# Performance work log

Hardware: AMD Instinct MI355X
Metric: run time of the kernel (lower is better)

## Reference

```python
import jax, jax.numpy as jnp
import numpy as np

NUM_HEADS = 8
NSCALE = 2  # len(sr_ratio) + 1 with sr_ratio=[2.0]


def setup_inputs() -> dict:
    key = jax.random.key(0)
    ks = jax.random.split(key, 12)
    B, Nq, Np, C, n_up, N_all = 16, 1024, 1024, 512, 2048, 4096
    s = C ** -0.5  # keep attention logits in a sane range
    return {
        "query": jax.random.normal(ks[0], (Nq, B, C), jnp.float32),
        "key": jax.random.normal(ks[1], (Np, B, C), jnp.float32),
        "key_pos": jax.random.uniform(ks[2], (B, Np, 3), jnp.float32),
        "xyz_all": jax.random.uniform(ks[3], (B, N_all, 3), jnp.float32),
        "xyz_upsample": jax.random.uniform(ks[4], (B, n_up, 3), jnp.float32),
        "Wq": jax.random.normal(ks[5], (C, C), jnp.float32) * s,
        "Wkv1": jax.random.normal(ks[6], (C, C), jnp.float32) * s,
        "Wkv2": jax.random.normal(ks[7], (C, C), jnp.float32) * s,
        "fp_w": jax.random.normal(ks[8], (C, C), jnp.float32) * s,
        "fp_b": jnp.zeros((C,), jnp.float32),
        "proj_w": jax.random.normal(ks[9], (C, C), jnp.float32) * s,
        "proj_b": jnp.zeros((C,), jnp.float32),
    }


def _fp_upsample(xyz_up, key_pos, key_feats, fp_w, fp_b):
    """PointnetFPModuleUpSample: 3-NN inverse-distance feature interpolation
    from Np known points (key_pos) onto n_up target points, followed by a
    pointwise MLP (1x1 conv, BN folded) + ReLU.
    key_feats: (Np, B, C) -> returns (B, n_up, C)."""
    d2 = jnp.sum((xyz_up[:, :, None, :] - key_pos[:, None, :, :]) ** 2, axis=-1)  # (B, n, Np)
    negd, idx = jax.lax.top_k(-d2, 3)  # 3 nearest neighbors, (B, n, 3)
    w = 1.0 / (-negd + 1e-8)
    w = w / jnp.sum(w, axis=-1, keepdims=True)
    feats = jnp.transpose(key_feats, (1, 0, 2))  # (B, Np, C)
    g = jnp.take_along_axis(feats[:, None, :, :], idx[..., None], axis=2)  # (B, n, 3, C)
    interp = jnp.sum(g * w[..., None], axis=2)  # (B, n, C)
    return jax.nn.relu(interp @ fp_w.T + fp_b)


def reference(query, key, key_pos, xyz_all, xyz_upsample,
              Wq, Wkv1, Wkv2, fp_w, fp_b, proj_w, proj_b):
    Np, B, C = key.shape
    Nq = query.shape[0]
    H = NUM_HEADS
    nh = H // NSCALE  # heads per scale group
    hd = C // H
    scale = hd ** -0.5

    # NOTE: torch reshapes (N,B,C) -> (B,N,...) WITHOUT permuting first; we
    # replicate the identical row-major reshape for bit-faithful structure.
    q = (query @ Wq.T).reshape(B, Nq, H, hd).transpose(0, 2, 1, 3)  # (B,H,Nq,hd)

    def attend(qs, kv):
        k, v = kv[0], kv[1]
        a = jax.nn.softmax(jnp.einsum('bhqd,bhkd->bhqk', qs, k) * scale, axis=-1)
        o = jnp.einsum('bhqk,bhkd->bhqd', a, v)
        return o.transpose(0, 2, 1, 3).reshape(B, Nq, nh * hd)

    # scale 1: full-resolution keys
    kv1 = (key @ Wkv1.T).reshape(B, -1, 2, nh, hd).transpose(2, 0, 3, 1, 4)
    x1 = attend(q[:, :nh], kv1)

    # scale 2: FP-upsampled keys (sr_ratio=2.0 -> 2*base_np points)
    key2 = _fp_upsample(xyz_upsample, key_pos, key, fp_w, fp_b)  # (B, n, C)
    key2_nbc = key2.transpose(1, 0, 2)  # (n, B, C), matches permute(2,0,1) of (B,C,n)
    kv2 = (key2_nbc @ Wkv2.T).reshape(B, -1, 2, nh, hd).transpose(2, 0, 3, 1, 4)
    x2 = attend(q[:, nh:], kv2)

    x = jnp.concatenate([x1, x2], axis=-1) @ proj_w.T + proj_b  # (B, Nq, C)
    return x.transpose(1, 0, 2)  # (Nq, B, C)
```

## Files before the change

### kernel.cpp

```cpp
#include <hip/hip_runtime.h>
#include <cstdint>
#include <cstddef>

#define CD   512
#define BDIM 16
#define NQ   1024
#define NP   1024
#define NUP  2048

typedef unsigned short u16;
typedef short short8 __attribute__((ext_vector_type(8)));
typedef float f32x4  __attribute__((ext_vector_type(4)));
typedef uint32_t u32x4 __attribute__((ext_vector_type(4)));

#define GLOAD16(g, l) __builtin_amdgcn_global_load_lds( \
    (const __attribute__((address_space(1))) void*)(g), \
    (__attribute__((address_space(3))) void*)(l), 16, 0, 0)

__device__ __forceinline__ u16 rne_bf16(float x) {
  uint32_t u = __float_as_uint(x);
  return (u16)((u + 0x7fffu + ((u >> 16) & 1u)) >> 16);
}
__device__ __forceinline__ float bf2f(u16 v) {
  return __uint_as_float(((uint32_t)v) << 16);
}

__global__ __launch_bounds__(256) void prep_kernel(
    const float* __restrict__ query, u16* __restrict__ Qa,
    const float* __restrict__ key, u16* __restrict__ Ka,
    const float* __restrict__ Wq, const float* __restrict__ Wkv1,
    const float* __restrict__ projw, const float* __restrict__ fpw,
    const float* __restrict__ wkv2, u16* __restrict__ Wq2,
    u16* __restrict__ Wkv12, u16* __restrict__ proj2,
    u16* __restrict__ fpwb, u16* __restrict__ wkv2b,
    const float* __restrict__ key_pos, const float* __restrict__ xyz_up,
    int* __restrict__ idx_out, float* __restrict__ w_out)
{
  const int bx = blockIdx.x;
  const int tid = threadIdx.x;
  if (bx < 8832) {
    const float* in; u16* out; float scl = 1.0f; long u;
    if (bx < 8192) {
      in = (bx < 4096) ? query : key;
      out = (bx < 4096) ? Qa : Ka;
      u = (long)(bx & 4095) * 256 + tid;
    } else {
      const int job = (bx - 8192) >> 7;
      in  = (job == 0) ? Wq  : (job == 1) ? Wkv1  : (job == 2) ? projw : (job == 3) ? fpw  : wkv2;
      out = (job == 0) ? Wq2 : (job == 1) ? Wkv12 : (job == 2) ? proj2 : (job == 3) ? fpwb : wkv2b;
      if (job == 0) scl = 0.18033688011112042f;
      u = (long)((bx - 8192) & 127) * 256 + tid;
    }
    const float* ip = in + u * 8;
    float v[8];
    *(float4*)&v[0] = *(const float4*)ip;
    *(float4*)&v[4] = *(const float4*)(ip + 4);
    short8 o;
#pragma unroll
    for (int i = 0; i < 8; ++i) o[i] = (short)rne_bf16(v[i] * scl);
    *(short8*)(out + u * 8) = o;
    return;
  }
  __shared__ __align__(16) float4 kp4[NP];
  const int kb = bx - 8832;
  const int b = kb >> 7;
  const int n0 = (kb & 127) * 16;
  const float* kpb = key_pos + (long)b * NP * 3;
#pragma unroll
  for (int s = 0; s < 4; ++s) {
    const int t = s * 256 + tid;
    kp4[t] = make_float4(kpb[t * 3], kpb[t * 3 + 1], kpb[t * 3 + 2], 0.0f);
  }
  __syncthreads();
  const int sc = tid & 15, pt = tid >> 4;
  const int n = n0 + pt;
  const float ux = xyz_up[(b * NUP + n) * 3 + 0];
  const float uy = xyz_up[(b * NUP + n) * 3 + 1];
  const float uz = xyz_up[(b * NUP + n) * 3 + 2];
  float e0 = 3.4e38f, e1 = 3.4e38f, e2 = 3.4e38f;
  int j0 = 0, j1 = 0, j2 = 0;
  for (int it = 0; it < 64; ++it) {
    const int j = it * 16 + sc;
    const float4 kv = kp4[j];
    const float dx = ux - kv.x, dy = uy - kv.y, dz = uz - kv.z;
    const float dd = dx * dx + dy * dy + dz * dz;
    if (dd < e2) {
      if (dd < e1) {
        e2 = e1; j2 = j1;
        if (dd < e0) { e1 = e0; j1 = j0; e0 = dd; j0 = j; }
        else         { e1 = dd; j1 = j; }
      } else { e2 = dd; j2 = j; }
    }
  }
#pragma unroll
  for (int ms = 1; ms <= 8; ms <<= 1) {
    const float pd0 = __shfl_xor(e0, ms), pd1 = __shfl_xor(e1, ms), pd2 = __shfl_xor(e2, ms);
    const int   pi0 = __shfl_xor(j0, ms), pi1 = __shfl_xor(j1, ms), pi2 = __shfl_xor(j2, ms);
    float cd[3] = {pd0, pd1, pd2};
    int   ci[3] = {pi0, pi1, pi2};
#pragma unroll
    for (int t = 0; t < 3; ++t) {
      const float dd = cd[t]; const int jj = ci[t];
      if (dd < e2 || (dd == e2 && jj < j2)) {
        if (dd < e1 || (dd == e1 && jj < j1)) {
          e2 = e1; j2 = j1;
          if (dd < e0 || (dd == e0 && jj < j0)) { e1 = e0; j1 = j0; e0 = dd; j0 = jj; }
          else                                  { e1 = dd; j1 = jj; }
        } else { e2 = dd; j2 = jj; }
      }
    }
  }
  if (sc == 0) {
    const float w0 = 1.0f / (e0 + 1e-8f);
    const float w1 = 1.0f / (e1 + 1e-8f);
    const float w2 = 1.0f / (e2 + 1e-8f);
    const float inv = 1.0f / ((w0 + w1) + w2);
    const long r = (long)b * NUP + n;
    idx_out[r * 3 + 0] = j0; idx_out[r * 3 + 1] = j1; idx_out[r * 3 + 2] = j2;
    w_out[r * 3 + 0] = w0 * inv; w_out[r * 3 + 1] = w1 * inv; w_out[r * 3 + 2] = w2 * inv;
  }
}

__global__ __launch_bounds__(256) void interp_bf16_kernel(
    const u16* __restrict__ Ka, const int* __restrict__ idx,
    const float* __restrict__ w, u16* __restrict__ out)
{
  const int t = threadIdx.x;
  const long r = (long)blockIdx.x * 4 + (t >> 6);
  const int j = t & 63;
  const int b = (int)(r >> 11);
  const int j0 = idx[r * 3 + 0], j1 = idx[r * 3 + 1], j2 = idx[r * 3 + 2];
  const float w0 = w[r * 3 + 0], w1 = w[r * 3 + 1], w2 = w[r * 3 + 2];
  const short8 a0 = *(const short8*)(Ka + ((long)j0 * BDIM + b) * CD + j * 8);
  const short8 a1 = *(const short8*)(Ka + ((long)j1 * BDIM + b) * CD + j * 8);
  const short8 a2 = *(const short8*)(Ka + ((long)j2 * BDIM + b) * CD + j * 8);
  short8 o;
#pragma unroll
  for (int i = 0; i < 8; ++i)
    o[i] = (short)rne_bf16(bf2f((u16)a0[i]) * w0 + bf2f((u16)a1[i]) * w1
                         + bf2f((u16)a2[i]) * w2);
  *(short8*)(out + r * CD + j * 8) = o;
}

template<int AMODE, int OMODE, int KE>
__device__ __forceinline__ void gemm_body64(
    u16* __restrict__ As, u16* __restrict__ Ws,
    const u16* __restrict__ A, const u16* __restrict__ W,
    const float* __restrict__ bias, void* __restrict__ outv,
    const int m0, const int n0)
{
  const int tid = threadIdx.x;
  const int lane = tid & 63, wv = tid >> 6;
  const int rch = tid & 7;

  f32x4 acc[4][4];
#pragma unroll
  for (int mi = 0; mi < 4; ++mi)
#pragma unroll
    for (int ni = 0; ni < 4; ++ni)
#pragma unroll
      for (int r = 0; r < 4; ++r) acc[mi][ni][r] = 0.0f;

  const long rowb = (long)KE * 2;
  const char* gA[4]; const char* gW[4];
#pragma unroll
  for (int s = 0; s < 4; ++s) {
    const int row = s * 32 + (tid >> 3);
    const int gm = m0 + row;
    const long arow = (AMODE == 0) ? (long)gm : (long)(gm & 15) * 2048 + (gm >> 4);
    const int kb0 = (rch ^ (row & 7)) << 4;
    gA[s] = (const char*)A + arow * rowb + kb0;
    gW[s] = (const char*)W + (long)(n0 + row) * rowb + kb0;
  }
  const int wr = (wv >> 1) * 64, wc = (wv & 1) * 64;
  const int g = lane >> 4, cl = lane & 15;

  for (int kt = 0; kt < KE / 64; ++kt) {
#pragma unroll
    for (int s = 0; s < 4; ++s) {
      GLOAD16(gA[s], (char*)As + (s * 256 + tid) * 16);
      GLOAD16(gW[s], (char*)Ws + (s * 256 + tid) * 16);
      gA[s] += 128; gW[s] += 128;
    }
    __syncthreads();
#pragma unroll
    for (int kb = 0; kb < 2; ++kb) {
      short8 af[4], bf[4];
#pragma unroll
      for (int i = 0; i < 4; ++i) {
        const int ra = wr + i * 16 + cl;
        af[i] = *(const short8*)((const char*)As + ra * 128
                 + ((kb * 64 + g * 16) ^ ((ra & 7) << 4)));
        const int rb = wc + i * 16 + cl;
        bf[i] = *(const short8*)((const char*)Ws + rb * 128
                 + ((kb * 64 + g * 16) ^ ((rb & 7) << 4)));
      }
#pragma unroll
      for (int mi = 0; mi < 4; ++mi)
#pragma unroll
        for (int ni = 0; ni < 4; ++ni)
          acc[mi][ni] = __builtin_amdgcn_mfma_f32_16x16x32_bf16(af[mi], bf[ni], acc[mi][ni], 0, 0, 0);
    }
    __syncthreads();
  }

#pragma unroll
  for (int mi = 0; mi < 4; ++mi)
#pragma unroll
    for (int ni = 0; ni < 4; ++ni)
#pragma unroll
      for (int r = 0; r < 4; ++r) {
        const int gm = m0 + wr + mi * 16 + g * 4 + r;
        const int gn = n0 + wc + ni * 16 + cl;
        float v = acc[mi][ni][r];
        if (OMODE == 0) {
          ((u16*)outv)[(long)gm * 512 + gn] = rne_bf16(v);
        } else if (OMODE == 1) {
          v = fmaxf(v + bias[gn], 0.0f);
          ((u16*)outv)[(long)gm * 512 + gn] = rne_bf16(v);
        } else {
          v += bias[gn];
          ((float*)outv)[((long)(gm & 1023) * BDIM + (gm >> 10)) * 512 + gn] = v;
        }
      }
}

__global__ __launch_bounds__(256) void gemm_mega_kernel(
    const u16* __restrict__ IN2, const u16* __restrict__ fpwb,
    const float* __restrict__ fp_b, u16* __restrict__ KEY2,
    const u16* __restrict__ Qa, const u16* __restrict__ Wq2, u16* __restrict__ Qb,
    const u16* __restrict__ Ka, const u16* __restrict__ Wkv12, u16* __restrict__ KV1)
{
  __shared__ __align__(16) u16 As[128 * 64];
  __shared__ __align__(16) u16 Ws[128 * 64];
  const int bid = blockIdx.x;
  if (bid < 1024) {
    gemm_body64<0, 1, 512>(As, Ws, IN2, fpwb, fp_b, KEY2, (bid >> 2) * 128, (bid & 3) * 128);
  } else if (bid < 1536) {
    const int t = bid - 1024;
    gemm_body64<0, 0, 512>(As, Ws, Qa, Wq2, nullptr, Qb, (t >> 2) * 128, (t & 3) * 128);
  } else {
    const int t = bid - 1536;
    gemm_body64<0, 0, 512>(As, Ws, Ka, Wkv12, nullptr, KV1, (t >> 2) * 128, (t & 3) * 128);
  }
}

__device__ __forceinline__ void transpose_body(
    u16* __restrict__ L, const u16* __restrict__ KV, u16* __restrict__ Vt,
    const int NK, const int kt, const int h, const int b)
{
  const int t = threadIdx.x;
  {
    const int n = t >> 2, d0 = (t & 3) * 16;
    const u16* src = KV + ((size_t)b * NK + kt * 64 + n) * 512 + 256 + h * 64 + d0;
    *(short8*)&L[n * 68 + d0] = *(const short8*)src;
    *(short8*)&L[n * 68 + d0 + 8] = *(const short8*)(src + 8);
  }
  __syncthreads();
  const int d = t >> 2, n0 = (t & 3) * 16;
  short8 o0, o1;
#pragma unroll
  for (int i = 0; i < 8; ++i) {
    o0[i] = (short)L[(n0 + i) * 68 + d];
    o1[i] = (short)L[(n0 + 8 + i) * 68 + d];
  }
  u16* dst = Vt + ((size_t)((b * 4 + h) * 64 + d)) * NK + kt * 64 + n0;
  *(short8*)dst = o0; *(short8*)(dst + 8) = o1;
}

__global__ __launch_bounds__(256) void gemm_kv2_vt1_kernel(
    const u16* __restrict__ KEY2, const u16* __restrict__ wkv2b,
    u16* __restrict__ KV2,
    const u16* __restrict__ KV1, u16* __restrict__ Vt1)
{
  __shared__ __align__(16) u16 As[128 * 64];
  __shared__ __align__(16) u16 Ws[128 * 64];
  const int bid = blockIdx.x;
  if (bid < 1024) {
    gemm_body64<1, 0, 512>(As, Ws, KEY2, wkv2b, nullptr, KV2,
                           (bid >> 2) * 128, (bid & 3) * 128);
  } else {
    const int tb = bid - 1024;
    transpose_body(As, KV1, Vt1, 1024, tb & 15, (tb >> 4) & 3, tb >> 6);
  }
}

__global__ __launch_bounds__(256) void vt2_kernel(
    const u16* __restrict__ KV2, u16* __restrict__ Vt2)
{
  __shared__ u16 L[64 * 68];
  transpose_body(L, KV2, Vt2, 2048, blockIdx.x, blockIdx.y, blockIdx.z);
}

__global__ __launch_bounds__(256) void gemm_proj64_kernel(
    const u16* __restrict__ A, const u16* __restrict__ W,
    const float* __restrict__ bias, float* __restrict__ out)
{
  __shared__ __align__(16) u16 As[64 * 32];
  __shared__ __align__(16) u16 Ws[128 * 32];
  const int tid = threadIdx.x;
  const int lane = tid & 63, wv = tid >> 6;
  const int m0 = blockIdx.x * 64, n0 = blockIdx.y * 128;

  f32x4 acc[2][4];
#pragma unroll
  for (int mi = 0; mi < 2; ++mi)
#pragma unroll
    for (int ni = 0; ni < 4; ++ni)
#pragma unroll
      for (int r = 0; r < 4; ++r) acc[mi][ni][r] = 0.0f;

  const int ar = tid >> 2, ac = tid & 3;
  const char* gA = (const char*)A + (long)(m0 + ar) * 1024 + ((ac ^ (ar & 3)) << 4);
  const char* gW[2];
#pragma unroll
  for (int s = 0; s < 2; ++s) {
    const int rw = s * 64 + ar;
    gW[s] = (const char*)W + (long)(n0 + rw) * 1024 + ((ac ^ (rw & 3)) << 4);
  }
  const int wr = (wv >> 1) * 32, wc = (wv & 1) * 64;
  const int g = lane >> 4, cl = lane & 15;
  const int gx = (g ^ (cl & 3)) << 4;

  for (int kt = 0; kt < 16; ++kt) {
    GLOAD16(gA, (char*)As + tid * 16); gA += 64;
#pragma unroll
    for (int s = 0; s < 2; ++s) {
      GLOAD16(gW[s], (char*)Ws + (s * 256 + tid) * 16); gW[s] += 64;
    }
    __syncthreads();
    short8 af[2], bf[4];
#pragma unroll
    for (int i = 0; i < 2; ++i)
      af[i] = *(const short8*)((const char*)As + (wr + i * 16 + cl) * 64 + gx);
#pragma unroll
    for (int j = 0; j < 4; ++j)
      bf[j] = *(const short8*)((const char*)Ws + (wc + j * 16 + cl) * 64 + gx);
#pragma unroll
    for (int mi = 0; mi < 2; ++mi)
#pragma unroll
      for (int ni = 0; ni < 4; ++ni)
        acc[mi][ni] = __builtin_amdgcn_mfma_f32_16x16x32_bf16(af[mi], bf[ni], acc[mi][ni], 0, 0, 0);
    __syncthreads();
  }

#pragma unroll
  for (int mi = 0; mi < 2; ++mi)
#pragma unroll
    for (int ni = 0; ni < 4; ++ni)
#pragma unroll
      for (int r = 0; r < 4; ++r) {
        const int gm = m0 + wr + mi * 16 + g * 4 + r;
        const int gn = n0 + wc + ni * 16 + cl;
        out[((long)(gm & 1023) * BDIM + (gm >> 10)) * 512 + gn] = acc[mi][ni][r] + bias[gn];
      }
}

template<int NK>
__device__ __forceinline__ void attn_body(
    u16* __restrict__ Ks, u16* __restrict__ Vs,
    const u16* __restrict__ Q, const u16* __restrict__ KV,
    const u16* __restrict__ Vt, u16* __restrict__ X,
    const int h, const int sc, const int qt, const int b)
{
  const int tid = threadIdx.x;
  const int lane = tid & 63, wv = tid >> 6;
  const int g = lane >> 4, cl = lane & 15;

  const u16* qptr = Q + ((size_t)(b * 1024 + qt * 64 + wv * 16 + cl)) * 512
                      + (sc * 4 + h) * 64 + g * 8;
  const short8 qf0 = *(const short8*)qptr;
  const short8 qf1 = *(const short8*)(qptr + 32);

  f32x4 acc[4];
#pragma unroll
  for (int dj = 0; dj < 4; ++dj)
#pragma unroll
    for (int r = 0; r < 4; ++r) acc[dj][r] = 0.0f;
  float l = 0.0f;

  const char* kB = (const char*)(KV + (size_t)b * NK * 512 + h * 64);
  const char* vB = (const char*)(Vt + (size_t)((b * 4 + h) * 64) * NK);
  uint32_t koffL[4], voffL[4];
#pragma unroll
  for (int s = 0; s < 4; ++s) {
    const int c = s * 256 + tid;
    { const int rr = c >> 3, ch = c & 7;
      const int sig = (rr & 3) | ((rr >> 1) & 4);
      koffL[s] = rr * 1024 + ((ch ^ sig) << 4); }
    { const int rr = c >> 4, ch = c & 15;
      voffL[s] = rr * (NK * 2) + ((ch ^ (rr & 7)) << 4); }
  }

  int koffb[2][2];
#pragma unroll
  for (int half = 0; half < 2; ++half) {
    const int rest = ((cl & 12) << 1) + half * 4 + (cl & 3);
    const int swz = ((rest & 3) << 4) | ((rest & 8) << 3);
#pragma unroll
    for (int dh = 0; dh < 2; ++dh)
      koffb[half][dh] = rest * 128 + ((dh * 64 + g * 16) ^ swz);
  }
  int voffx[4][2];
#pragma unroll
  for (int dj = 0; dj < 4; ++dj) {
    const int vrow = dj * 16 + cl;
    const int base = vrow * 256 + ((g * 16) ^ ((vrow & 7) << 4));
    voffx[dj][0] = base; voffx[dj][1] = base ^ 64;
  }
  const int srcb = (lane & 48) | (g << 2);

  for (int kt = 0; kt < NK / 128; ++kt) {
    const char* kT = kB + (size_t)kt * 131072;
    const char* vT = vB + (size_t)kt * 256;
#pragma unroll
    for (int s = 0; s < 4; ++s) {
      GLOAD16(kT + koffL[s], (char*)Ks + s * 4096 + tid * 16);
      GLOAD16(vT + voffL[s], (char*)Vs + s * 4096 + tid * 16);
    }
    __syncthreads();

    f32x4 sv[8];
#pragma unroll
    for (int f = 0; f < 8; ++f)
#pragma unroll
      for (int r = 0; r < 4; ++r) sv[f][r] = 0.0f;
    __builtin_amdgcn_s_setprio(1);
#pragma unroll
    for (int ks = 0; ks < 4; ++ks)
#pragma unroll
      for (int half = 0; half < 2; ++half) {
        const int f = ks * 2 + half;
        const short8 ak0 = *(const short8*)((const char*)Ks + ks * 4096 + koffb[half][0]);
        const short8 ak1 = *(const short8*)((const char*)Ks + ks * 4096 + koffb[half][1]);
        sv[f] = __builtin_amdgcn_mfma_f32_16x16x32_bf16(ak0, qf0, sv[f], 0, 0, 0);
        sv[f] = __builtin_amdgcn_mfma_f32_16x16x32_bf16(ak1, qf1, sv[f], 0, 0, 0);
      }
    __builtin_amdgcn_s_setprio(0);

    float rs = 0.0f;
#pragma unroll
    for (int f = 0; f < 8; ++f)
#pragma unroll
      for (int r = 0; r < 4; ++r) {
        sv[f][r] = __builtin_amdgcn_exp2f(sv[f][r]);
        rs += sv[f][r];
      }
    rs += __shfl_xor(rs, 16);
    rs += __shfl_xor(rs, 32);
    l += rs;

    u32x4 pw[4];
#pragma unroll
    for (int ks = 0; ks < 4; ++ks) {
      asm("v_cvt_pk_bf16_f32 %0, %1, %2" : "=v"(pw[ks][0]) : "v"(sv[2*ks][0]),   "v"(sv[2*ks][1]));
      asm("v_cvt_pk_bf16_f32 %0, %1, %2" : "=v"(pw[ks][1]) : "v"(sv[2*ks][2]),   "v"(sv[2*ks][3]));
      asm("v_cvt_pk_bf16_f32 %0, %1, %2" : "=v"(pw[ks][2]) : "v"(sv[2*ks+1][0]), "v"(sv[2*ks+1][1]));
      asm("v_cvt_pk_bf16_f32 %0, %1, %2" : "=v"(pw[ks][3]) : "v"(sv[2*ks+1][2]), "v"(sv[2*ks+1][3]));
    }

    __builtin_amdgcn_s_setprio(1);
#pragma unroll
    for (int ks = 0; ks < 4; ++ks) {
      const short8 pa = __builtin_bit_cast(short8, pw[ks]);
#pragma unroll
      for (int dj = 0; dj < 4; ++dj) {
        const short8 bv = *(const short8*)((const char*)Vs +
                          ((ks >> 1) * 128 + voffx[dj][ks & 1]));
        acc[dj] = __builtin_amdgcn_mfma_f32_16x16x32_bf16(pa, bv, acc[dj], 0, 0, 0);
      }
    }
    __builtin_amdgcn_s_setprio(0);
    __syncthreads();
  }

  const float inv = 1.0f / l;
  float invr[4];
#pragma unroll
  for (int r = 0; r < 4; ++r) invr[r] = __shfl(inv, srcb | r);
#pragma unroll
  for (int dj = 0; dj < 4; ++dj)
#pragma unroll
    for (int r = 0; r < 4; ++r) {
      const long gq = b * 1024 + qt * 64 + wv * 16 + g * 4 + r;
      X[gq * 512 + sc * 256 + h * 64 + dj * 16 + cl] = rne_bf16(acc[dj][r] * invr[r]);
    }
}

__global__ __launch_bounds__(256, 4) void attn_fused_kernel(
    const u16* __restrict__ Q,
    const u16* __restrict__ KV1, const u16* __restrict__ KV2,
    const u16* __restrict__ Vt1, const u16* __restrict__ Vt2,
    u16* __restrict__ X)
{
  __shared__ __align__(16) u16 Ks[128 * 64];
  __shared__ __align__(16) u16 Vs[64 * 128];
  const int d = blockIdx.x + (blockIdx.y << 4) + (blockIdx.z << 8);
  const int qt = (d >> 3) & 15;
  const int grp = (d & 7) + ((d >> 7) << 3);
  const int b = grp & 15, z = grp >> 4;
  if (z < 4) attn_body<1024>(Ks, Vs, Q, KV1, Vt1, X, z, 0, qt, b);
  else       attn_body<2048>(Ks, Vs, Q, KV2, Vt2, X, z - 4, 1, qt, b);
}

extern "C" void kernel_launch(void* const* d_in, const int* in_sizes, int n_in,
                              void* d_out, int out_size, void* d_ws, size_t ws_size,
                              hipStream_t stream) {
  const float* query   = (const float*)d_in[0];
  const float* key     = (const float*)d_in[1];
  const float* key_pos = (const float*)d_in[2];
  const float* xyz_up  = (const float*)d_in[4];
  const float* Wq      = (const float*)d_in[5];
  const float* Wkv1    = (const float*)d_in[6];
  const float* Wkv2    = (const float*)d_in[7];
  const float* fp_w    = (const float*)d_in[8];
  const float* fp_b    = (const float*)d_in[9];
  const float* proj_w  = (const float*)d_in[10];
  const float* proj_b  = (const float*)d_in[11];

  char* ws = (char*)d_ws;
  const size_t MB = 1024 * 1024;
  u16*  Qa    = (u16*)(ws + 0);
  u16*  Ka    = (u16*)(ws + 16 * MB);
  u16*  Qb    = (u16*)(ws + 32 * MB);
  u16*  KV1   = (u16*)(ws + 48 * MB);
  u16*  IN2   = (u16*)(ws + 64 * MB);
  u16*  KEY2  = (u16*)(ws + 96 * MB);
  u16*  Vt1   = (u16*)(ws + 128 * MB);
  u16*  Vt2   = (u16*)(ws + 136 * MB);
  u16*  Wq2   = (u16*)(ws + 152 * MB);
  u16*  Wkv12 = (u16*)(ws + 152 * MB + 512 * 1024);
  u16*  proj2 = (u16*)(ws + 153 * MB);
  u16*  fpwb  = (u16*)(ws + 153 * MB + 512 * 1024);
  u16*  wkv2b = (u16*)(ws + 154 * MB);
  int*  idxb  = (int*)(ws + 155 * MB);
  float* wb   = (float*)(ws + 156 * MB);
  u16*  KV2   = IN2;
  u16*  X     = Qa;

  prep_kernel<<<dim3(10880), 256, 0, stream>>>(
      query, Qa, key, Ka, Wq, Wkv1, proj_w, fp_w, Wkv2,
      Wq2, Wkv12, proj2, fpwb, wkv2b, key_pos, xyz_up, idxb, wb);
  interp_bf16_kernel<<<dim3(8192), 256, 0, stream>>>(Ka, idxb, wb, IN2);
  gemm_mega_kernel<<<dim3(2048), 256, 0, stream>>>(
      IN2, fpwb, fp_b, KEY2, Qa, Wq2, Qb, Ka, Wkv12, KV1);
  gemm_kv2_vt1_kernel<<<dim3(2048), 256, 0, stream>>>(KEY2, wkv2b, KV2, KV1, Vt1);
  vt2_kernel<<<dim3(32, 4, 16), 256, 0, stream>>>(KV2, Vt2);
  attn_fused_kernel<<<dim3(16, 16, 8), 256, 0, stream>>>(Qb, KV1, KV2, Vt1, Vt2, X);
  gemm_proj64_kernel<<<dim3(256, 4), 256, 0, stream>>>(X, proj2, proj_b, (float*)d_out);
}
```

Before: 234.3 us.

## Fuse V transposes into GEMM epilogues, regroup kernels, double-buffer attention loads

The GEMM epilogue gains a mode that transposes the V half of the KV projection through shared memory and writes Vt directly. This removes the standalone transpose passes over KV1 and KV2. The interpolation gather is merged into the Q/KV1 GEMM launch, and the FP GEMM becomes its own launch, so the kernel sequence shrinks. The attention loop now issues the next K and V tile loads early, using explicit waitcnt and barrier calls, so they overlap with compute; this adds hand-managed synchronisation that could be fragile.

```diff
diff --git a/kernel.cpp b/kernel.cpp
--- a/kernel.cpp
+++ b/kernel.cpp
@@ -121,33 +121,12 @@
   }
 }
 
-__global__ __launch_bounds__(256) void interp_bf16_kernel(
-    const u16* __restrict__ Ka, const int* __restrict__ idx,
-    const float* __restrict__ w, u16* __restrict__ out)
-{
-  const int t = threadIdx.x;
-  const long r = (long)blockIdx.x * 4 + (t >> 6);
-  const int j = t & 63;
-  const int b = (int)(r >> 11);
-  const int j0 = idx[r * 3 + 0], j1 = idx[r * 3 + 1], j2 = idx[r * 3 + 2];
-  const float w0 = w[r * 3 + 0], w1 = w[r * 3 + 1], w2 = w[r * 3 + 2];
-  const short8 a0 = *(const short8*)(Ka + ((long)j0 * BDIM + b) * CD + j * 8);
-  const short8 a1 = *(const short8*)(Ka + ((long)j1 * BDIM + b) * CD + j * 8);
-  const short8 a2 = *(const short8*)(Ka + ((long)j2 * BDIM + b) * CD + j * 8);
-  short8 o;
-#pragma unroll
-  for (int i = 0; i < 8; ++i)
-    o[i] = (short)rne_bf16(bf2f((u16)a0[i]) * w0 + bf2f((u16)a1[i]) * w1
-                         + bf2f((u16)a2[i]) * w2);
-  *(short8*)(out + r * CD + j * 8) = o;
-}
-
-template<int AMODE, int OMODE, int KE>
+template<int AMODE, int OMODE, int KE, int NKT>
 __device__ __forceinline__ void gemm_body64(
     u16* __restrict__ As, u16* __restrict__ Ws,
     const u16* __restrict__ A, const u16* __restrict__ W,
     const float* __restrict__ bias, void* __restrict__ outv,
-    const int m0, const int n0)
+    u16* __restrict__ Vt, const int m0, const int n0)
 {
   const int tid = threadIdx.x;
   const int lane = tid & 63, wv = tid >> 6;
@@ -204,92 +183,123 @@
     __syncthreads();
   }
 
-#pragma unroll
-  for (int mi = 0; mi < 4; ++mi)
-#pragma unroll
-    for (int ni = 0; ni < 4; ++ni)
-#pragma unroll
-      for (int r = 0; r < 4; ++r) {
-        const int gm = m0 + wr + mi * 16 + g * 4 + r;
-        const int gn = n0 + wc + ni * 16 + cl;
-        float v = acc[mi][ni][r];
-        if (OMODE == 0) {
-          ((u16*)outv)[(long)gm * 512 + gn] = rne_bf16(v);
-        } else if (OMODE == 1) {
-          v = fmaxf(v + bias[gn], 0.0f);
-          ((u16*)outv)[(long)gm * 512 + gn] = rne_bf16(v);
-        } else {
-          v += bias[gn];
-          ((float*)outv)[((long)(gm & 1023) * BDIM + (gm >> 10)) * 512 + gn] = v;
+  if constexpr (OMODE == 3) {
+    u16* T = As;
+#pragma unroll
+    for (int ni = 0; ni < 4; ++ni) {
+      const int n = wc + ni * 16 + cl;
+      const int swz = (n & 15) << 4;
+      const int rb2 = n * 256;
+#pragma unroll
+      for (int mi = 0; mi < 4; ++mi) {
+        uint32_t lo, hi;
+        asm("v_cvt_pk_bf16_f32 %0, %1, %2" : "=v"(lo) : "v"(acc[mi][ni][0]), "v"(acc[mi][ni][1]));
+        asm("v_cvt_pk_bf16_f32 %0, %1, %2" : "=v"(hi) : "v"(acc[mi][ni][2]), "v"(acc[mi][ni][3]));
+        const int m2 = 2 * (wr + mi * 16 + g * 4);
+        uint2 pk; pk.x = lo; pk.y = hi;
+        *(uint2*)((char*)T + rb2 + (m2 ^ swz)) = pk;
+      }
+    }
+    __syncthreads();
+    const int nl = tid >> 1, mh = tid & 1;
+    const int v = (n0 - 256) + nl;
+    const int hh = v >> 6, dd = v & 63;
+    const int bq = m0 / NKT;
+    const int p0 = (m0 & (NKT - 1)) + mh * 64;
+    u16* dst = Vt + ((size_t)((bq * 4 + hh) * 64 + dd)) * NKT + p0;
+    const int swz = (nl & 15) << 4;
+#pragma unroll
+    for (int j = 0; j < 8; ++j) {
+      const int m2 = mh * 128 + j * 16;
+      const short8 val = *(const short8*)((const char*)T + nl * 256 + (m2 ^ swz));
+      *(short8*)(dst + j * 8) = val;
+    }
+    return;
+  } else {
+#pragma unroll
+    for (int mi = 0; mi < 4; ++mi)
+#pragma unroll
+      for (int ni = 0; ni < 4; ++ni)
+#pragma unroll
+        for (int r = 0; r < 4; ++r) {
+          const int gm = m0 + wr + mi * 16 + g * 4 + r;
+          const int gn = n0 + wc + ni * 16 + cl;
+          float vv = acc[mi][ni][r];
+          if (OMODE == 0) {
+            ((u16*)outv)[(long)gm * 512 + gn] = rne_bf16(vv);
+          } else if (OMODE == 1) {
+            vv = fmaxf(vv + bias[gn], 0.0f);
+            ((u16*)outv)[(long)gm * 512 + gn] = rne_bf16(vv);
+          } else {
+            vv += bias[gn];
+            ((float*)outv)[((long)(gm & 1023) * BDIM + (gm >> 10)) * 512 + gn] = vv;
+          }
         }
-      }
-}
-
-__global__ __launch_bounds__(256) void gemm_mega_kernel(
-    const u16* __restrict__ IN2, const u16* __restrict__ fpwb,
-    const float* __restrict__ fp_b, u16* __restrict__ KEY2,
+  }
+}
+
+template<int AMODE, int OMODE, int KE>
+__global__ __launch_bounds__(256) void gemm_one(
+    const u16* __restrict__ A, const u16* __restrict__ W,
+    const float* __restrict__ bias, void* __restrict__ outv)
+{
+  __shared__ __align__(16) u16 SH[16384];
+  gemm_body64<AMODE, OMODE, KE, 1024>(SH, SH + 8192, A, W, bias, outv, nullptr,
+                                      blockIdx.x * 128, blockIdx.y * 128);
+}
+
+__global__ __launch_bounds__(256) void qkv1_interp_kernel(
     const u16* __restrict__ Qa, const u16* __restrict__ Wq2, u16* __restrict__ Qb,
-    const u16* __restrict__ Ka, const u16* __restrict__ Wkv12, u16* __restrict__ KV1)
-{
-  __shared__ __align__(16) u16 As[128 * 64];
-  __shared__ __align__(16) u16 Ws[128 * 64];
+    const u16* __restrict__ Ka, const u16* __restrict__ Wkv12,
+    u16* __restrict__ KV1, u16* __restrict__ Vt1,
+    const int* __restrict__ idx, const float* __restrict__ w, u16* __restrict__ IN2)
+{
+  __shared__ __align__(16) u16 SH[16384];
   const int bid = blockIdx.x;
-  if (bid < 1024) {
-    gemm_body64<0, 1, 512>(As, Ws, IN2, fpwb, fp_b, KEY2, (bid >> 2) * 128, (bid & 3) * 128);
-  } else if (bid < 1536) {
-    const int t = bid - 1024;
-    gemm_body64<0, 0, 512>(As, Ws, Qa, Wq2, nullptr, Qb, (t >> 2) * 128, (t & 3) * 128);
+  if (bid < 512) {
+    gemm_body64<0, 0, 512, 1024>(SH, SH + 8192, Qa, Wq2, nullptr, Qb, nullptr,
+                                 (bid >> 2) * 128, (bid & 3) * 128);
+  } else if (bid < 1024) {
+    const int t = bid - 512;
+    const int n0 = (t & 3) * 128;
+    if (n0 >= 256)
+      gemm_body64<0, 3, 512, 1024>(SH, SH + 8192, Ka, Wkv12, nullptr, KV1, Vt1,
+                                   (t >> 2) * 128, n0);
+    else
+      gemm_body64<0, 0, 512, 1024>(SH, SH + 8192, Ka, Wkv12, nullptr, KV1, nullptr,
+                                   (t >> 2) * 128, n0);
   } else {
-    const int t = bid - 1536;
-    gemm_body64<0, 0, 512>(As, Ws, Ka, Wkv12, nullptr, KV1, (t >> 2) * 128, (t & 3) * 128);
-  }
-}
-
-__device__ __forceinline__ void transpose_body(
-    u16* __restrict__ L, const u16* __restrict__ KV, u16* __restrict__ Vt,
-    const int NK, const int kt, const int h, const int b)
-{
-  const int t = threadIdx.x;
-  {
-    const int n = t >> 2, d0 = (t & 3) * 16;
-    const u16* src = KV + ((size_t)b * NK + kt * 64 + n) * 512 + 256 + h * 64 + d0;
-    *(short8*)&L[n * 68 + d0] = *(const short8*)src;
-    *(short8*)&L[n * 68 + d0 + 8] = *(const short8*)(src + 8);
-  }
-  __syncthreads();
-  const int d = t >> 2, n0 = (t & 3) * 16;
-  short8 o0, o1;
-#pragma unroll
-  for (int i = 0; i < 8; ++i) {
-    o0[i] = (short)L[(n0 + i) * 68 + d];
-    o1[i] = (short)L[(n0 + 8 + i) * 68 + d];
-  }
-  u16* dst = Vt + ((size_t)((b * 4 + h) * 64 + d)) * NK + kt * 64 + n0;
-  *(short8*)dst = o0; *(short8*)(dst + 8) = o1;
-}
-
-__global__ __launch_bounds__(256) void gemm_kv2_vt1_kernel(
+    const int t = threadIdx.x;
+    const long r = (long)(bid - 1024) * 4 + (t >> 6);
+    const int j = t & 63;
+    const int b = (int)(r >> 11);
+    const int j0 = idx[r * 3 + 0], j1 = idx[r * 3 + 1], j2 = idx[r * 3 + 2];
+    const float w0 = w[r * 3 + 0], w1 = w[r * 3 + 1], w2 = w[r * 3 + 2];
+    const short8 a0 = *(const short8*)(Ka + ((long)j0 * BDIM + b) * CD + j * 8);
+    const short8 a1 = *(const short8*)(Ka + ((long)j1 * BDIM + b) * CD + j * 8);
+    const short8 a2 = *(const short8*)(Ka + ((long)j2 * BDIM + b) * CD + j * 8);
+    short8 o;
+#pragma unroll
+    for (int i = 0; i < 8; ++i)
+      o[i] = (short)rne_bf16(bf2f((u16)a0[i]) * w0 + bf2f((u16)a1[i]) * w1
+                           + bf2f((u16)a2[i]) * w2);
+    *(short8*)(IN2 + r * CD + j * 8) = o;
+  }
+}
+
+__global__ __launch_bounds__(256) void kv2_kernel(
     const u16* __restrict__ KEY2, const u16* __restrict__ wkv2b,
-    u16* __restrict__ KV2,
-    const u16* __restrict__ KV1, u16* __restrict__ Vt1)
-{
-  __shared__ __align__(16) u16 As[128 * 64];
-  __shared__ __align__(16) u16 Ws[128 * 64];
-  const int bid = blockIdx.x;
-  if (bid < 1024) {
-    gemm_body64<1, 0, 512>(As, Ws, KEY2, wkv2b, nullptr, KV2,
-                           (bid >> 2) * 128, (bid & 3) * 128);
-  } else {
-    const int tb = bid - 1024;
-    transpose_body(As, KV1, Vt1, 1024, tb & 15, (tb >> 4) & 3, tb >> 6);
-  }
-}
-
-__global__ __launch_bounds__(256) void vt2_kernel(
-    const u16* __restrict__ KV2, u16* __restrict__ Vt2)
-{
-  __shared__ u16 L[64 * 68];
-  transpose_body(L, KV2, Vt2, 2048, blockIdx.x, blockIdx.y, blockIdx.z);
+    u16* __restrict__ KV2, u16* __restrict__ Vt2)
+{
+  __shared__ __align__(16) u16 SH[16384];
+  const int t = blockIdx.x;
+  const int n0 = (t & 3) * 128;
+  if (n0 >= 256)
+    gemm_body64<1, 3, 512, 2048>(SH, SH + 8192, KEY2, wkv2b, nullptr, KV2, Vt2,
+                                 (t >> 2) * 128, n0);
+  else
+    gemm_body64<1, 0, 512, 2048>(SH, SH + 8192, KEY2, wkv2b, nullptr, KV2, nullptr,
+                                 (t >> 2) * 128, n0);
 }
 
 __global__ __launch_bounds__(256) void gemm_proj64_kernel(
@@ -410,15 +420,22 @@
   }
   const int srcb = (lane & 48) | (g << 2);
 
-  for (int kt = 0; kt < NK / 128; ++kt) {
-    const char* kT = kB + (size_t)kt * 131072;
-    const char* vT = vB + (size_t)kt * 256;
-#pragma unroll
-    for (int s = 0; s < 4; ++s) {
-      GLOAD16(kT + koffL[s], (char*)Ks + s * 4096 + tid * 16);
-      GLOAD16(vT + voffL[s], (char*)Vs + s * 4096 + tid * 16);
-    }
-    __syncthreads();
+  constexpr int NT = NK / 128;
+#define ISSUE_K(kt_) { const char* kT_ = kB + (size_t)(kt_) * 131072; \
+  _Pragma("unroll") for (int s_ = 0; s_ < 4; ++s_) \
+    GLOAD16(kT_ + koffL[s_], (char*)Ks + s_ * 4096 + tid * 16); }
+#define ISSUE_V(kt_) { const char* vT_ = vB + (size_t)(kt_) * 256; \
+  _Pragma("unroll") for (int s_ = 0; s_ < 4; ++s_) \
+    GLOAD16(vT_ + voffL[s_], (char*)Vs + s_ * 4096 + tid * 16); }
+
+  asm volatile("s_waitcnt vmcnt(0)" ::: "memory");
+  ISSUE_K(0);
+  ISSUE_V(0);
+
+  for (int kt = 0; kt < NT; ++kt) {
+    asm volatile("s_waitcnt vmcnt(4)" ::: "memory");
+    __builtin_amdgcn_s_barrier();
+    __builtin_amdgcn_sched_barrier(0);
 
     f32x4 sv[8];
 #pragma unroll
@@ -438,6 +455,11 @@
       }
     __builtin_amdgcn_s_setprio(0);
 
+    asm volatile("s_waitcnt lgkmcnt(0)" ::: "memory");
+    __builtin_amdgcn_s_barrier();
+    __builtin_amdgcn_sched_barrier(0);
+    if (kt + 1 < NT) { ISSUE_K(kt + 1); }
+
     float rs = 0.0f;
 #pragma unroll
     for (int f = 0; f < 8; ++f)
@@ -459,6 +481,11 @@
       asm("v_cvt_pk_bf16_f32 %0, %1, %2" : "=v"(pw[ks][3]) : "v"(sv[2*ks+1][2]), "v"(sv[2*ks+1][3]));
     }
 
+    if (kt + 1 < NT) { asm volatile("s_waitcnt vmcnt(4)" ::: "memory"); }
+    else             { asm volatile("s_waitcnt vmcnt(0)" ::: "memory"); }
+    __builtin_amdgcn_s_barrier();
+    __builtin_amdgcn_sched_barrier(0);
+
     __builtin_amdgcn_s_setprio(1);
 #pragma unroll
     for (int ks = 0; ks < 4; ++ks) {
@@ -471,8 +498,14 @@
       }
     }
     __builtin_amdgcn_s_setprio(0);
-    __syncthreads();
-  }
+
+    asm volatile("s_waitcnt lgkmcnt(0)" ::: "memory");
+    __builtin_amdgcn_s_barrier();
+    __builtin_amdgcn_sched_barrier(0);
+    if (kt + 1 < NT) { ISSUE_V(kt + 1); }
+  }
+#undef ISSUE_K
+#undef ISSUE_V
 
   const float inv = 1.0f / l;
   float invr[4];
@@ -541,11 +574,10 @@
   prep_kernel<<<dim3(10880), 256, 0, stream>>>(
       query, Qa, key, Ka, Wq, Wkv1, proj_w, fp_w, Wkv2,
       Wq2, Wkv12, proj2, fpwb, wkv2b, key_pos, xyz_up, idxb, wb);
-  interp_bf16_kernel<<<dim3(8192), 256, 0, stream>>>(Ka, idxb, wb, IN2);
-  gemm_mega_kernel<<<dim3(2048), 256, 0, stream>>>(
-      IN2, fpwb, fp_b, KEY2, Qa, Wq2, Qb, Ka, Wkv12, KV1);
-  gemm_kv2_vt1_kernel<<<dim3(2048), 256, 0, stream>>>(KEY2, wkv2b, KV2, KV1, Vt1);
-  vt2_kernel<<<dim3(32, 4, 16), 256, 0, stream>>>(KV2, Vt2);
+  qkv1_interp_kernel<<<dim3(9216), 256, 0, stream>>>(
+      Qa, Wq2, Qb, Ka, Wkv12, KV1, Vt1, idxb, wb, IN2);
+  gemm_one<0, 1, 512><<<dim3(256, 4), 256, 0, stream>>>(IN2, fpwb, fp_b, KEY2);
+  kv2_kernel<<<dim3(1024), 256, 0, stream>>>(KEY2, wkv2b, KV2, Vt2);
   attn_fused_kernel<<<dim3(16, 16, 8), 256, 0, stream>>>(Qb, KV1, KV2, Vt1, Vt2, X);
   gemm_proj64_kernel<<<dim3(256, 4), 256, 0, stream>>>(X, proj2, proj_b, (float*)d_out);
 }
```

Measured after the change: 234.3 us. About the same (+0.0%).
